# Performance work log

Measured on AMD Instinct MI355X. Metric: run time of the kernel, lower is better.

## Reference

```python
import jax, jax.numpy as jnp
import numpy as np
import math

C_S, C_Z = 384, 128
N_HEAD, C = 12, 16
N_QP, N_PV = 4, 8
B, N_RES = 1, 384


def quat_to_rot(q):
    # q: (..., 4) unnormalized quaternion -> (..., 3, 3) rotation matrix
    q = q / jnp.linalg.norm(q, axis=-1, keepdims=True)
    w, x, y, z = q[..., 0], q[..., 1], q[..., 2], q[..., 3]
    R = jnp.stack([
        1 - 2 * (y * y + z * z), 2 * (x * y - w * z), 2 * (x * z + w * y),
        2 * (x * y + w * z), 1 - 2 * (x * x + z * z), 2 * (y * z - w * x),
        2 * (x * z - w * y), 2 * (y * z + w * x), 1 - 2 * (x * x + y * y),
    ], axis=-1)
    return R.reshape(q.shape[:-1] + (3, 3))


def warp_3d_point(T, p):
    # T: (..., 1, 1, N, 4, 4) rigid transforms; p: (..., H, P, N, 3)
    R = T[..., :3, :3]
    t = T[..., :3, 3]
    return jnp.squeeze(R @ p[..., None], -1) + t


def warp_3d_point_inv(T, p):
    # Inverse rigid transform: R^T (p - t)
    R = T[..., :3, :3]
    t = T[..., :3, 3]
    return jnp.squeeze(jnp.swapaxes(R, -1, -2) @ (p - t)[..., None], -1)


def setup_inputs() -> dict:
    key = jax.random.key(0)
    ks = jax.random.split(key, 24)
    s = jax.random.normal(ks[0], (B, N_RES, C_S), dtype=jnp.float32)
    z = jax.random.normal(ks[1], (B, N_RES, N_RES, C_Z), dtype=jnp.float32)
    # Build rigid backbone transforms T (rotation from random quaternion + translation)
    quat = jax.random.normal(ks[2], (B, N_RES, 4), dtype=jnp.float32)
    trans = jax.random.normal(ks[3], (B, N_RES, 3), dtype=jnp.float32) * 10.0
    R = quat_to_rot(quat)
    T = jnp.zeros((B, N_RES, 4, 4), dtype=jnp.float32)
    T = T.at[..., :3, :3].set(R)
    T = T.at[..., :3, 3].set(trans)
    T = T.at[..., 3, 3].set(1.0)

    def lin(k, din, dout):
        kw, kb = jax.random.split(k)
        W = jax.random.normal(kw, (din, dout), dtype=jnp.float32) * 0.02
        b = jax.random.normal(kb, (dout,), dtype=jnp.float32) * 0.01
        return W, b

    Wq, bq = lin(ks[4], C_S, N_HEAD * C)
    Wk, bk = lin(ks[5], C_S, N_HEAD * C)
    Wv, bv = lin(ks[6], C_S, N_HEAD * C)
    Wqp, bqp = lin(ks[7], C_S, 3 * N_QP * N_HEAD)
    Wkp, bkp = lin(ks[8], C_S, 3 * N_QP * N_HEAD)
    Wvp, bvp = lin(ks[9], C_S, 3 * N_PV * N_HEAD)
    Wb, bb = lin(ks[10], C_Z, N_HEAD)
    d_out_in = N_HEAD * C_Z + N_HEAD * C + N_HEAD * 4 * N_PV
    Wo, bo = lin(ks[11], d_out_in, C_S)
    head_weights = jax.random.normal(ks[12], (N_HEAD,), dtype=jnp.float32) * 0.1
    return dict(s=s, z=z, T=T, Wq=Wq, bq=bq, Wk=Wk, bk=bk, Wv=Wv, bv=bv,
                Wqp=Wqp, bqp=bqp, Wkp=Wkp, bkp=bkp, Wvp=Wvp, bvp=bvp,
                Wb=Wb, bb=bb, Wo=Wo, bo=bo, head_weights=head_weights)


def ipa_forward(s, z, T, Wq, bq, Wk, bk, Wv, bv, Wqp, bqp, Wkp, bkp,
                Wvp, bvp, Wb, bb, Wo, bo, head_weights):
    batch = s.shape[:-2]
    n = s.shape[-2]
    # --- prepare qkv ---
    def heads(x):  # (..., N, H*C) -> (..., H, N, C)
        return jnp.moveaxis(x.reshape(batch + (n, N_HEAD, C)), -3, -2)
    q = heads(s @ Wq + bq)
    k = heads(s @ Wk + bk)
    v = heads(s @ Wv + bv)

    def pts(x, P):  # (..., N, 3*H*P) -> (..., H, P, N, 3)
        x = x.reshape(batch + (n, 3, N_HEAD, P))
        return jnp.moveaxis(x, (-4, -3), (-2, -1))
    qp = pts(s @ Wqp + bqp, N_QP)
    kp = pts(s @ Wkp + bkp, N_QP)
    vp = pts(s @ Wvp + bvp, N_PV)

    # --- attention scores (Alg 22 line 7) ---
    wc = math.sqrt(2.0 / (9.0 * N_QP))
    wl = math.sqrt(1.0 / 3.0)
    gamma = jax.nn.softplus(head_weights).reshape(-1, 1, 1)  # (H,1,1)
    q = q * (1.0 / math.sqrt(C))
    bias = jnp.moveaxis(z @ Wb + bb, -1, -3)  # (..., H, N, N)
    qk = jnp.einsum('...hic,...hjc->...hij', q, k)
    T_bc = T.reshape(batch + (1, 1, n, 4, 4))
    tqp = warp_3d_point(T_bc, qp)[..., :, None, :]   # (..., H, QP, N, 1, 3)
    tkp = warp_3d_point(T_bc, kp)[..., None, :, :]   # (..., H, QP, 1, N, 3)
    sq_dist = jnp.sum((tqp - tkp) ** 2, axis=-1)      # (..., H, QP, N, N)
    qpkp_term = gamma * (wc / 2.0) * jnp.sum(sq_dist, axis=-3)  # (..., H, N, N)
    att = jax.nn.softmax(wl * (qk + bias - qpkp_term), axis=-1)

    # --- outputs ---
    pairwise = jnp.einsum('...ijc,...hij->...hic', z, att)
    pairwise = jnp.moveaxis(pairwise, -3, -2).reshape(batch + (n, N_HEAD * C_Z))
    v_out = jnp.einsum('...hij,...hjc->...hic', att, v)
    v_out = jnp.moveaxis(v_out, -3, -2).reshape(batch + (n, N_HEAD * C))
    vt = warp_3d_point(T_bc, vp)                                # (..., H, PV, N, 3)
    v_att = jnp.einsum('...hij,...hkjp->...hkip', att, vt)     # (..., H, PV, N, 3)
    v_tr = warp_3d_point_inv(T_bc, v_att)                       # (..., H, PV, N, 3)
    v_tr = jnp.einsum('...hpic->...ichp', v_tr)                 # (..., N, 3, H, PV)
    norm = jnp.linalg.norm(v_tr, axis=-3, keepdims=True)        # (..., N, 1, H, PV)
    vp_norm = norm.reshape(batch + (n, N_HEAD * N_PV))
    vp_out = v_tr.reshape(batch + (n, 3 * N_HEAD * N_PV))

    out = jnp.concatenate([v_out, vp_out, vp_norm, pairwise], axis=-1)
    return out @ Wo + bo


def reference(s, z, T, Wq, bq, Wk, bk, Wv, bv, Wqp, bqp, Wkp, bkp,
              Wvp, bvp, Wb, bb, Wo, bo, head_weights):
    return ipa_forward(s, z, T, Wq, bq, Wk, bk, Wv, bv, Wqp, bqp, Wkp, bkp,
                       Wvp, bvp, Wb, bb, Wo, bo, head_weights)
```

## Files before the change

### kernel.cpp

```cpp
#include <hip/hip_runtime.h>
#include <math.h>

#define NRES 384
#define NH   12
#define WLc 0.5773502691896258f
#define WCc 0.23570226039551587f

typedef __attribute__((ext_vector_type(8))) _Float16 half8;
typedef __attribute__((ext_vector_type(2))) _Float16 half2v;
typedef __attribute__((ext_vector_type(4))) float f32x4;

#define OFF_P    0
#define OFF_SH   442368
#define OFF_WCT  516096
#define OFF_BCT  737280
#define OFF_QE   738432
#define OFF_KE   885888
#define OFF_VET  1033344
#define OFF_WOT  1143936
#define OFF_CAT  1549440
#define OFF_ATT  1954944
#define OFF_BIAS 2839680

__global__ __launch_bounds__(256) void pack_bias(
    const float* __restrict__ s,  const float* __restrict__ z,
    const float* __restrict__ Wq,  const float* __restrict__ bq,
    const float* __restrict__ Wk,  const float* __restrict__ bk,
    const float* __restrict__ Wv,  const float* __restrict__ bv,
    const float* __restrict__ Wqp, const float* __restrict__ bqp,
    const float* __restrict__ Wkp, const float* __restrict__ bkp,
    const float* __restrict__ Wvp, const float* __restrict__ bvp,
    const float* __restrict__ Wb,  const float* __restrict__ bb,
    const float* __restrict__ Wo,
    float* __restrict__ ws)
{
    int b = blockIdx.x, t = threadIdx.x;
    __shared__ float tile[64 * 65];
    __shared__ _Float16 wbT[16 * 136];
    __shared__ float sbb[16];

    if (b >= 451) {
        _Float16* biasb = (_Float16*)(ws + OFF_BIAS);
        int bi = b - 451;
        size_t m0 = (size_t)bi * 64;
        if (t < 128) {
            #pragma unroll
            for (int h = 0; h < 12; h++) wbT[h * 136 + t] = (_Float16)(WLc * Wb[t * 12 + h]);
            #pragma unroll
            for (int h = 12; h < 16; h++) wbT[h * 136 + t] = (_Float16)0.f;
        }
        if (t < 16) sbb[t] = (t < 12) ? WLc * bb[t] : 0.f;
        __syncthreads();
        int w = t >> 6, lane = t & 63;
        int m = lane & 15, q = lane >> 4;
        size_t ri = m0 + w * 16 + m;
        const float* zr = z + ri * 128 + q * 8;
        f32x4 acc = {0};
        #pragma unroll
        for (int sI = 0; sI < 4; sI++) {
            float4 v0 = *(const float4*)(zr + sI * 32);
            float4 v1 = *(const float4*)(zr + sI * 32 + 4);
            half8 a;
            a[0]=(_Float16)v0.x; a[1]=(_Float16)v0.y; a[2]=(_Float16)v0.z; a[3]=(_Float16)v0.w;
            a[4]=(_Float16)v1.x; a[5]=(_Float16)v1.y; a[6]=(_Float16)v1.z; a[7]=(_Float16)v1.w;
            half8 bf = *(const half8*)(wbT + m * 136 + sI * 32 + q * 8);
            acc = __builtin_amdgcn_mfma_f32_16x16x32_f16(a, bf, acc, 0, 0, 0);
        }
        if (m < 12) {
            #pragma unroll
            for (int r = 0; r < 4; r++)
                biasb[(size_t)m * 147456 + m0 + w * 16 + q * 4 + r] = (_Float16)(acc[r] + sbb[m]);
        }
        return;
    }

    _Float16* sh  = (_Float16*)(ws + OFF_SH);
    _Float16* wct = (_Float16*)(ws + OFF_WCT);
    _Float16* wot = (_Float16*)(ws + OFF_WOT);
    float* bct = ws + OFF_BCT;

    if (b < 144) {
        int id = b * 256 + t;
        float4 v = ((const float4*)s)[id];
        _Float16 r[4] = { (_Float16)v.x, (_Float16)v.y, (_Float16)v.z, (_Float16)v.w };
        *(uint2*)(sh + id * 4) = *(uint2*)r;
        return;
    }
    if (b < 252) {
        int ti = b - 144;
        int k0 = (ti % 6) * 64, n0 = (ti / 6) * 64;
        int cl = t & 63, rg = t >> 6;
        int ncat = n0 + cl;
        const float* W; int dout, col;
        if      (ncat < 192) { W = Wq;  dout = 192; col = ncat; }
        else if (ncat < 384) { W = Wk;  dout = 192; col = ncat - 192; }
        else if (ncat < 576) { W = Wv;  dout = 192; col = ncat - 384; }
        else if (ncat < 720) { W = Wqp; dout = 144; col = ncat - 576; }
        else if (ncat < 864) { W = Wkp; dout = 144; col = ncat - 720; }
        else                 { W = Wvp; dout = 288; col = ncat - 864; }
        #pragma unroll
        for (int u = 0; u < 16; u++) {
            int r = rg * 16 + u;
            tile[r * 65 + cl] = W[(size_t)(k0 + r) * dout + col];
        }
        __syncthreads();
        #pragma unroll
        for (int u2 = 0; u2 < 2; u2++) {
            int item = t + 256 * u2;
            int nl = item >> 3, kg = item & 7;
            half8 rr;
            #pragma unroll
            for (int jj = 0; jj < 8; jj++) rr[jj] = (_Float16)tile[(kg * 8 + jj) * 65 + nl];
            *(half8*)(wct + (size_t)(n0 + nl) * 384 + k0 + kg * 8) = rr;
        }
        return;
    }
    if (b < 450) {
        int ti = b - 252;
        int k0 = (ti % 33) * 64, n0 = (ti / 33) * 64;
        int cl = t & 63, rg = t >> 6;
        #pragma unroll
        for (int u = 0; u < 16; u++) {
            int r = rg * 16 + u;
            tile[r * 65 + cl] = Wo[(size_t)(k0 + r) * 384 + n0 + cl];
        }
        __syncthreads();
        #pragma unroll
        for (int u2 = 0; u2 < 2; u2++) {
            int item = t + 256 * u2;
            int nl = item >> 3, kg = item & 7;
            half8 rr;
            #pragma unroll
            for (int jj = 0; jj < 8; jj++) rr[jj] = (_Float16)tile[(kg * 8 + jj) * 65 + nl];
            *(half8*)(wot + (size_t)(n0 + nl) * 2112 + k0 + kg * 8) = rr;
        }
        return;
    }
    for (int e = t; e < 1152; e += 256) {
        float bv_;
        if      (e < 192) bv_ = bq[e];
        else if (e < 384) bv_ = bk[e - 192];
        else if (e < 576) bv_ = bv[e - 384];
        else if (e < 720) bv_ = bqp[e - 576];
        else if (e < 864) bv_ = bkp[e - 720];
        else              bv_ = bvp[e - 864];
        bct[e] = bv_;
    }
}

__global__ __launch_bounds__(256) void proj_mfma(float* __restrict__ ws)
{
    const _Float16* sh  = (const _Float16*)(ws + OFF_SH);
    const _Float16* wct = (const _Float16*)(ws + OFF_WCT);
    const float* bct = ws + OFF_BCT;
    float* P = ws + OFF_P;

    __shared__ float sAcc[2][16][65];

    int t = threadIdx.x, w = t >> 6, lane = t & 63;
    int m = lane & 15, q = lane >> 4;
    int mh = w & 1, kh = w >> 1;
    int n0 = blockIdx.x * 64, m0 = blockIdx.y * 32 + mh * 16;

    f32x4 acc[4] = {0};
    const _Float16* arow = sh + (size_t)(m0 + m) * 384 + kh * 192;
    #pragma unroll 3
    for (int s = 0; s < 6; s++) {
        int k = s * 32 + q * 8;
        half8 a = *(const half8*)(arow + k);
        #pragma unroll
        for (int nt = 0; nt < 4; nt++) {
            half8 b = *(const half8*)(wct + (size_t)(n0 + nt * 16 + m) * 384 + kh * 192 + k);
            acc[nt] = __builtin_amdgcn_mfma_f32_16x16x32_f16(a, b, acc[nt], 0, 0, 0);
        }
    }
    if (kh == 0) {
        #pragma unroll
        for (int nt = 0; nt < 4; nt++)
            #pragma unroll
            for (int r = 0; r < 4; r++)
                sAcc[mh][q * 4 + r][nt * 16 + m] = acc[nt][r];
    }
    __syncthreads();
    if (kh == 1) {
        #pragma unroll
        for (int nt = 0; nt < 4; nt++) {
            int col = n0 + nt * 16 + m;
            float bias = bct[col];
            #pragma unroll
            for (int r = 0; r < 4; r++)
                P[(size_t)(m0 + q * 4 + r) * 1152 + col] =
                    acc[nt][r] + sAcc[mh][q * 4 + r][nt * 16 + m] + bias;
        }
    }
}

__global__ __launch_bounds__(192) void prep_kernel(
    const float* __restrict__ T, const float* __restrict__ hw,
    float* __restrict__ ws)
{
    int i = blockIdx.x, t = threadIdx.x;
    const float* pr = ws + OFF_P + (size_t)i * 1152;
    float* Qe = ws + OFF_QE;
    float* Ke = ws + OFF_KE;
    _Float16* vet = (_Float16*)(ws + OFF_VET);

    __shared__ float sT[16], sG[12];
    __shared__ float sTQ[12][4][3], sTK[12][4][3];
    if (t < 16) sT[t] = T[i * 16 + t];
    if (t < 12) { float x = hw[t]; sG[t] = (x > 20.f) ? x : log1pf(__expf(x)); }
    __syncthreads();
    float R00=sT[0],R01=sT[1],R02=sT[2],t0=sT[3];
    float R10=sT[4],R11=sT[5],R12=sT[6],t1=sT[7];
    float R20=sT[8],R21=sT[9],R22=sT[10],t2=sT[11];

    if (t < 48) {
        int h = t >> 2, p = t & 3;
        float a0 = pr[576 + 0*48 + h*4 + p], a1 = pr[576 + 1*48 + h*4 + p], a2 = pr[576 + 2*48 + h*4 + p];
        sTQ[h][p][0] = R00*a0 + R01*a1 + R02*a2 + t0;
        sTQ[h][p][1] = R10*a0 + R11*a1 + R12*a2 + t1;
        sTQ[h][p][2] = R20*a0 + R21*a1 + R22*a2 + t2;
    } else if (t < 96) {
        int tt = t - 48, h = tt >> 2, p = tt & 3;
        float a0 = pr[720 + 0*48 + h*4 + p], a1 = pr[720 + 1*48 + h*4 + p], a2 = pr[720 + 2*48 + h*4 + p];
        sTK[h][p][0] = R00*a0 + R01*a1 + R02*a2 + t0;
        sTK[h][p][1] = R10*a0 + R11*a1 + R12*a2 + t1;
        sTK[h][p][2] = R20*a0 + R21*a1 + R22*a2 + t2;
    } else {
        int tt = t - 96, h = tt >> 3, p = tt & 7;
        float a0 = pr[864 + 0*96 + h*8 + p], a1 = pr[864 + 1*96 + h*8 + p], a2 = pr[864 + 2*96 + h*8 + p];
        vet[(size_t)(h*48 + 16 + p*3 + 0) * 384 + i] = (_Float16)(R00*a0 + R01*a1 + R02*a2 + t0);
        vet[(size_t)(h*48 + 16 + p*3 + 1) * 384 + i] = (_Float16)(R10*a0 + R11*a1 + R12*a2 + t1);
        vet[(size_t)(h*48 + 16 + p*3 + 2) * 384 + i] = (_Float16)(R20*a0 + R21*a1 + R22*a2 + t2);
    }
    {
        int h = t >> 4, c = t & 15;
        vet[(size_t)(h*48 + c) * 384 + i] = (_Float16)pr[384 + h*16 + c];
        if (t < 96) vet[(size_t)((t>>3)*48 + 40 + (t&7)) * 384 + i] = (_Float16)0.f;
        Qe[(size_t)i*384 + h*32 + c] = WLc * 0.25f * pr[h*16 + c];
        Ke[((size_t)h*384 + i)*32 + c] = pr[192 + h*16 + c];
    }
    __syncthreads();
    if (t < 144) {
        int h = t / 12, d = t % 12, p = d / 3, r = d % 3;
        float gw = WLc * sG[h] * WCc;
        Qe[(size_t)i*384 + h*32 + 16 + d] = gw * sTQ[h][p][r];
        Ke[((size_t)h*384 + i)*32 + 16 + d] = sTK[h][p][r];
    }
    if (t < 12) {
        int h = t;
        float sqq = 0.f, sqk = 0.f;
        #pragma unroll
        for (int p = 0; p < 4; p++)
            #pragma unroll
            for (int r = 0; r < 3; r++) { sqq += sTQ[h][p][r]*sTQ[h][p][r]; sqk += sTK[h][p][r]*sTK[h][p][r]; }
        float gw = WLc * sG[h] * WCc;
        Qe[(size_t)i*384 + h*32 + 28] = -0.5f * gw;
        Qe[(size_t)i*384 + h*32 + 29] = -0.5f * gw * sqq;
        Qe[(size_t)i*384 + h*32 + 30] = 0.f;
        Qe[(size_t)i*384 + h*32 + 31] = 0.f;
        Ke[((size_t)h*384 + i)*32 + 28] = sqk;
        Ke[((size_t)h*384 + i)*32 + 29] = 1.f;
        Ke[((size_t)h*384 + i)*32 + 30] = 0.f;
        Ke[((size_t)h*384 + i)*32 + 31] = 0.f;
    }
}

__global__ __launch_bounds__(512) void logits_out40(
    const float* __restrict__ T, float* __restrict__ ws)
{
    __shared__ float sQe[8 * 32];
    __shared__ float sLg[8][384];
    __shared__ float sMS[16];
    __shared__ _Float16 sAttL[8 * 392];
    __shared__ float sO[8 * 49];
    __shared__ float sT8[8 * 16];

    int h = blockIdx.y, i0 = blockIdx.x * 8;
    int t = threadIdx.x;
    const float* Qe = ws + OFF_QE;
    const float* Ke = ws + OFF_KE;
    const _Float16* biasb = (const _Float16*)(ws + OFF_BIAS);
    const _Float16* vet = (const _Float16*)(ws + OFF_VET);
    _Float16* attg = (_Float16*)(ws + OFF_ATT);
    _Float16* catb = (_Float16*)(ws + OFF_CAT);

    if (t < 256)
        sQe[t] = Qe[(size_t)(i0 + (t >> 5)) * 384 + h * 32 + (t & 31)];
    if (t < 128)
        sT8[t] = T[(size_t)(i0 + (t >> 4)) * 16 + (t & 15)];
    __syncthreads();

    float lgv[8];
    if (t < 384) {
        int j = t;
        float ke[32];
        const float4* kr = (const float4*)(Ke + ((size_t)h * 384 + j) * 32);
        #pragma unroll
        for (int u = 0; u < 8; u++) { float4 v = kr[u]; ke[u*4]=v.x; ke[u*4+1]=v.y; ke[u*4+2]=v.z; ke[u*4+3]=v.w; }
        #pragma unroll
        for (int ii = 0; ii < 8; ii++) {
            float acc = (float)biasb[(size_t)h * 147456 + (size_t)(i0 + ii) * 384 + j];
            #pragma unroll
            for (int c = 0; c < 32; c++) acc += sQe[ii * 32 + c] * ke[c];
            lgv[ii] = acc;
            sLg[ii][j] = acc;
        }
    }
    __syncthreads();
    {
        int w = t >> 6, lane = t & 63;
        float vv[6], mx = -1e30f;
        #pragma unroll
        for (int u = 0; u < 6; u++) { vv[u] = sLg[w][lane + 64 * u]; mx = fmaxf(mx, vv[u]); }
        #pragma unroll
        for (int off = 1; off < 64; off <<= 1) mx = fmaxf(mx, __shfl_xor(mx, off));
        float sm = 0.f;
        #pragma unroll
        for (int u = 0; u < 6; u++) sm += __expf(vv[u] - mx);
        #pragma unroll
        for (int off = 1; off < 64; off <<= 1) sm += __shfl_xor(sm, off);
        if (lane == 0) { sMS[w] = mx; sMS[8 + w] = sm; }
    }
    __syncthreads();
    if (t < 384) {
        int j = t;
        #pragma unroll
        for (int ii = 0; ii < 8; ii++) {
            float a = __expf(lgv[ii] - sMS[ii]) * (1.0f / sMS[8 + ii]);
            attg[((size_t)h * 384 + i0 + ii) * 384 + j] = (_Float16)a;
            sAttL[ii * 392 + j] = (_Float16)a;
        }
    }
    __syncthreads();

    int w = t >> 6, lane = t & 63;
    int m16 = lane & 15, q = lane >> 4;
    if (w < 3) {
        int nt = w;
        f32x4 acc = {0};
        #pragma unroll 3
        for (int s = 0; s < 12; s++) {
            int k = s * 32 + q * 8;
            half8 a;
            if (m16 < 8) a = *(const half8*)(sAttL + m16 * 392 + k);
            else         a = (half8){0,0,0,0,0,0,0,0};
            half8 bfr = *(const half8*)(vet + (size_t)(h * 48 + nt * 16 + m16) * 384 + k);
            acc = __builtin_amdgcn_mfma_f32_16x16x32_f16(a, bfr, acc, 0, 0, 0);
        }
        #pragma unroll
        for (int r = 0; r < 4; r++) {
            int row = q * 4 + r;
            if (row < 8) sO[row * 49 + nt * 16 + m16] = acc[r];
        }
    }
    __syncthreads();

    if (t < 128) {
        int il = t >> 4, c = t & 15;
        catb[(size_t)(i0 + il) * 2112 + h * 16 + c] = (_Float16)sO[il * 49 + c];
    }
    if (t < 64) {
        int il = t >> 3, p = t & 7;
        const float* o = sO + il * 49 + 16 + p * 3;
        const float* Ti = sT8 + il * 16;
        float x0 = o[0] - Ti[3], x1 = o[1] - Ti[7], x2 = o[2] - Ti[11];
        float r0 = Ti[0]*x0 + Ti[4]*x1 + Ti[8]*x2;
        float r1 = Ti[1]*x0 + Ti[5]*x1 + Ti[9]*x2;
        float r2 = Ti[2]*x0 + Ti[6]*x1 + Ti[10]*x2;
        _Float16* cr = catb + (size_t)(i0 + il) * 2112;
        cr[192 + 0*96 + h*8 + p] = (_Float16)r0;
        cr[192 + 1*96 + h*8 + p] = (_Float16)r1;
        cr[192 + 2*96 + h*8 + p] = (_Float16)r2;
        cr[480 + h*8 + p] = (_Float16)sqrtf(r0*r0 + r1*r1 + r2*r2);
    }
}

__global__ __launch_bounds__(256) void pairwise_mfma(
    const float* __restrict__ z, float* __restrict__ ws)
{
    __shared__ _Float16 ztT[128 * 136];
    __shared__ __attribute__((aligned(16))) _Float16 sPW[1536];
    int i = blockIdx.x;
    int t = threadIdx.x, w = t >> 6, lane = t & 63;
    int m16 = lane & 15, q = lane >> 4;
    const _Float16* attg = (const _Float16*)(ws + OFF_ATT);
    _Float16* catb = (_Float16*)(ws + OFF_CAT);

    f32x4 acc0 = {0}, acc1 = {0};
    const _Float16* arow = attg + ((size_t)(m16 < 12 ? m16 : 0) * 384 + i) * 384;

    int cq = t & 31, g = t >> 5;
    for (int jc = 0; jc < 3; jc++) {
        if (jc) __syncthreads();
        const float* zb = z + ((size_t)i * 384 + jc * 128) * 128;
        #pragma unroll
        for (int jp = 0; jp < 8; jp++) {
            int j = g * 16 + jp * 2;
            float4 v0 = *(const float4*)(zb + (size_t)j * 128 + cq * 4);
            float4 v1 = *(const float4*)(zb + (size_t)(j + 1) * 128 + cq * 4);
            half2v c0 = {(_Float16)v0.x, (_Float16)v1.x};
            half2v c1 = {(_Float16)v0.y, (_Float16)v1.y};
            half2v c2 = {(_Float16)v0.z, (_Float16)v1.z};
            half2v c3 = {(_Float16)v0.w, (_Float16)v1.w};
            *(half2v*)(ztT + (cq * 4 + 0) * 136 + j) = c0;
            *(half2v*)(ztT + (cq * 4 + 1) * 136 + j) = c1;
            *(half2v*)(ztT + (cq * 4 + 2) * 136 + j) = c2;
            *(half2v*)(ztT + (cq * 4 + 3) * 136 + j) = c3;
        }
        __syncthreads();
        #pragma unroll
        for (int ks = 0; ks < 4; ks++) {
            int k = ks * 32 + q * 8;
            half8 a;
            if (m16 < 12) a = *(const half8*)(arow + jc * 128 + k);
            else          a = (half8){0,0,0,0,0,0,0,0};
            half8 b0 = *(const half8*)(ztT + (w * 32 + m16) * 136 + k);
            half8 b1 = *(const half8*)(ztT + (w * 32 + 16 + m16) * 136 + k);
            acc0 = __builtin_amdgcn_mfma_f32_16x16x32_f16(a, b0, acc0, 0, 0, 0);
            acc1 = __builtin_amdgcn_mfma_f32_16x16x32_f16(a, b1, acc1, 0, 0, 0);
        }
    }
    if (q < 3) {
        #pragma unroll
        for (int r = 0; r < 4; r++) {
            int h = q * 4 + r;
            sPW[h * 128 + w * 32 + m16]      = (_Float16)acc0[r];
            sPW[h * 128 + w * 32 + 16 + m16] = (_Float16)acc1[r];
        }
    }
    __syncthreads();
    if (t < 192)
        *(half8*)(catb + (size_t)i * 2112 + 576 + t * 8) = *(const half8*)(sPW + t * 8);
}

__global__ __launch_bounds__(256) void outgemm_mfma(
    float* __restrict__ ws, const float* __restrict__ bo, float* __restrict__ out)
{
    const _Float16* catb = (const _Float16*)(ws + OFF_CAT);
    const _Float16* wot = (const _Float16*)(ws + OFF_WOT);

    __shared__ float sAcc[2][16][65];

    int t = threadIdx.x, w = t >> 6, lane = t & 63;
    int m = lane & 15, q = lane >> 4;
    int mh = w & 1, kh = w >> 1;
    int n0 = blockIdx.x * 64;
    int m0 = blockIdx.y * 32 + mh * 16;

    f32x4 acc[4] = {0};
    int row = m0 + m;
    const _Float16* ar = catb + (size_t)row * 2112 + kh * 1056;
    #pragma unroll 3
    for (int s = 0; s < 33; s++) {
        int k = s * 32 + q * 8;
        half8 a = *(const half8*)(ar + k);
        #pragma unroll
        for (int nt = 0; nt < 4; nt++) {
            half8 b = *(const half8*)(wot + (size_t)(n0 + nt * 16 + m) * 2112 + kh * 1056 + k);
            acc[nt] = __builtin_amdgcn_mfma_f32_16x16x32_f16(a, b, acc[nt], 0, 0, 0);
        }
    }
    if (kh == 0) {
        #pragma unroll
        for (int nt = 0; nt < 4; nt++)
            #pragma unroll
            for (int r = 0; r < 4; r++)
                sAcc[mh][q * 4 + r][nt * 16 + m] = acc[nt][r];
    }
    __syncthreads();
    if (kh == 1) {
        #pragma unroll
        for (int nt = 0; nt < 4; nt++) {
            int col = n0 + nt * 16 + m;
            float bv = bo[col];
            #pragma unroll
            for (int r = 0; r < 4; r++)
                out[(size_t)(m0 + q * 4 + r) * 384 + col] =
                    acc[nt][r] + sAcc[mh][q * 4 + r][nt * 16 + m] + bv;
        }
    }
}

extern "C" void kernel_launch(void* const* d_in, const int* in_sizes, int n_in,
                              void* d_out, int out_size, void* d_ws, size_t ws_size,
                              hipStream_t stream)
{
    const float* s   = (const float*)d_in[0];
    const float* z   = (const float*)d_in[1];
    const float* T   = (const float*)d_in[2];
    const float* Wq  = (const float*)d_in[3];
    const float* bq  = (const float*)d_in[4];
    const float* Wk  = (const float*)d_in[5];
    const float* bk  = (const float*)d_in[6];
    const float* Wv  = (const float*)d_in[7];
    const float* bv  = (const float*)d_in[8];
    const float* Wqp = (const float*)d_in[9];
    const float* bqp = (const float*)d_in[10];
    const float* Wkp = (const float*)d_in[11];
    const float* bkp = (const float*)d_in[12];
    const float* Wvp = (const float*)d_in[13];
    const float* bvp = (const float*)d_in[14];
    const float* Wb  = (const float*)d_in[15];
    const float* bb  = (const float*)d_in[16];
    const float* Wo  = (const float*)d_in[17];
    const float* bo  = (const float*)d_in[18];
    const float* hw  = (const float*)d_in[19];
    float* ws  = (float*)d_ws;
    float* out = (float*)d_out;

    pack_bias<<<2755, 256, 0, stream>>>(s, z, Wq, bq, Wk, bk, Wv, bv,
                                        Wqp, bqp, Wkp, bkp, Wvp, bvp, Wb, bb, Wo, ws);
    proj_mfma<<<dim3(18, 12), 256, 0, stream>>>(ws);
    prep_kernel<<<384, 192, 0, stream>>>(T, hw, ws);
    logits_out40<<<dim3(48, 12), 512, 0, stream>>>(T, ws);
    pairwise_mfma<<<384, 256, 0, stream>>>(z, ws);
    outgemm_mfma<<<dim3(6, 12), 256, 0, stream>>>(ws, bo, out);
}
```

Measured before the change: 215.0 us.

## Fuse bias, logits, softmax, value and pairwise stages into one per-row kernel

```diff
diff --git a/kernel.cpp b/kernel.cpp
--- a/kernel.cpp
+++ b/kernel.cpp
@@ -19,60 +19,20 @@
 #define OFF_VET  1033344
 #define OFF_WOT  1143936
 #define OFF_CAT  1549440
-#define OFF_ATT  1954944
-#define OFF_BIAS 2839680
-
-__global__ __launch_bounds__(256) void pack_bias(
-    const float* __restrict__ s,  const float* __restrict__ z,
+
+__global__ __launch_bounds__(256) void pack_weights(
+    const float* __restrict__ s,
     const float* __restrict__ Wq,  const float* __restrict__ bq,
     const float* __restrict__ Wk,  const float* __restrict__ bk,
     const float* __restrict__ Wv,  const float* __restrict__ bv,
     const float* __restrict__ Wqp, const float* __restrict__ bqp,
     const float* __restrict__ Wkp, const float* __restrict__ bkp,
     const float* __restrict__ Wvp, const float* __restrict__ bvp,
-    const float* __restrict__ Wb,  const float* __restrict__ bb,
     const float* __restrict__ Wo,
     float* __restrict__ ws)
 {
     int b = blockIdx.x, t = threadIdx.x;
     __shared__ float tile[64 * 65];
-    __shared__ _Float16 wbT[16 * 136];
-    __shared__ float sbb[16];
-
-    if (b >= 451) {
-        _Float16* biasb = (_Float16*)(ws + OFF_BIAS);
-        int bi = b - 451;
-        size_t m0 = (size_t)bi * 64;
-        if (t < 128) {
-            #pragma unroll
-            for (int h = 0; h < 12; h++) wbT[h * 136 + t] = (_Float16)(WLc * Wb[t * 12 + h]);
-            #pragma unroll
-            for (int h = 12; h < 16; h++) wbT[h * 136 + t] = (_Float16)0.f;
-        }
-        if (t < 16) sbb[t] = (t < 12) ? WLc * bb[t] : 0.f;
-        __syncthreads();
-        int w = t >> 6, lane = t & 63;
-        int m = lane & 15, q = lane >> 4;
-        size_t ri = m0 + w * 16 + m;
-        const float* zr = z + ri * 128 + q * 8;
-        f32x4 acc = {0};
-        #pragma unroll
-        for (int sI = 0; sI < 4; sI++) {
-            float4 v0 = *(const float4*)(zr + sI * 32);
-            float4 v1 = *(const float4*)(zr + sI * 32 + 4);
-            half8 a;
-            a[0]=(_Float16)v0.x; a[1]=(_Float16)v0.y; a[2]=(_Float16)v0.z; a[3]=(_Float16)v0.w;
-            a[4]=(_Float16)v1.x; a[5]=(_Float16)v1.y; a[6]=(_Float16)v1.z; a[7]=(_Float16)v1.w;
-            half8 bf = *(const half8*)(wbT + m * 136 + sI * 32 + q * 8);
-            acc = __builtin_amdgcn_mfma_f32_16x16x32_f16(a, bf, acc, 0, 0, 0);
-        }
-        if (m < 12) {
-            #pragma unroll
-            for (int r = 0; r < 4; r++)
-                biasb[(size_t)m * 147456 + m0 + w * 16 + q * 4 + r] = (_Float16)(acc[r] + sbb[m]);
-        }
-        return;
-    }
 
     _Float16* sh  = (_Float16*)(ws + OFF_SH);
     _Float16* wct = (_Float16*)(ws + OFF_WCT);
@@ -266,53 +226,102 @@
     }
 }
 
-__global__ __launch_bounds__(512) void logits_out40(
-    const float* __restrict__ T, float* __restrict__ ws)
+__global__ __launch_bounds__(256) void flash_ipa(
+    const float* __restrict__ z, const float* __restrict__ T,
+    const float* __restrict__ Wb, const float* __restrict__ bb,
+    float* __restrict__ ws)
 {
-    __shared__ float sQe[8 * 32];
-    __shared__ float sLg[8][384];
-    __shared__ float sMS[16];
-    __shared__ _Float16 sAttL[8 * 392];
-    __shared__ float sO[8 * 49];
-    __shared__ float sT8[8 * 16];
-
-    int h = blockIdx.y, i0 = blockIdx.x * 8;
-    int t = threadIdx.x;
+    __shared__ __attribute__((aligned(16))) char uB[34816];
+    __shared__ __attribute__((aligned(16))) _Float16 pL[12 * 392];
+    __shared__ _Float16 wbT[16 * 136];
+    __shared__ float sTl[16];
+    __shared__ float sOL[12 * 49];
+    __shared__ __attribute__((aligned(16))) _Float16 sPW[1536];
+
+    float* lgL = (float*)uB;
+    _Float16* ztT = (_Float16*)uB;
+
+    int i = blockIdx.x, t = threadIdx.x;
+    int w = t >> 6, lane = t & 63;
+    int m16 = lane & 15, q = lane >> 4;
+
     const float* Qe = ws + OFF_QE;
     const float* Ke = ws + OFF_KE;
-    const _Float16* biasb = (const _Float16*)(ws + OFF_BIAS);
     const _Float16* vet = (const _Float16*)(ws + OFF_VET);
-    _Float16* attg = (_Float16*)(ws + OFF_ATT);
     _Float16* catb = (_Float16*)(ws + OFF_CAT);
 
-    if (t < 256)
-        sQe[t] = Qe[(size_t)(i0 + (t >> 5)) * 384 + h * 32 + (t & 31)];
-    if (t < 128)
-        sT8[t] = T[(size_t)(i0 + (t >> 4)) * 16 + (t & 15)];
-    __syncthreads();
-
-    float lgv[8];
-    if (t < 384) {
-        int j = t;
-        float ke[32];
-        const float4* kr = (const float4*)(Ke + ((size_t)h * 384 + j) * 32);
-        #pragma unroll
-        for (int u = 0; u < 8; u++) { float4 v = kr[u]; ke[u*4]=v.x; ke[u*4+1]=v.y; ke[u*4+2]=v.z; ke[u*4+3]=v.w; }
-        #pragma unroll
-        for (int ii = 0; ii < 8; ii++) {
-            float acc = (float)biasb[(size_t)h * 147456 + (size_t)(i0 + ii) * 384 + j];
-            #pragma unroll
-            for (int c = 0; c < 32; c++) acc += sQe[ii * 32 + c] * ke[c];
-            lgv[ii] = acc;
-            sLg[ii][j] = acc;
-        }
-    }
-    __syncthreads();
-    {
-        int w = t >> 6, lane = t & 63;
+    if (t < 16) sTl[t] = T[i * 16 + t];
+    if (t >= 192) {
+        int t2 = t - 192;
+        #pragma unroll
+        for (int cc = 0; cc < 2; cc++) {
+            int col = t2 * 2 + cc;
+            #pragma unroll
+            for (int h = 0; h < 12; h++) wbT[h * 136 + col] = (_Float16)(WLc * Wb[col * 12 + h]);
+            #pragma unroll
+            for (int h = 12; h < 16; h++) wbT[h * 136 + col] = (_Float16)0.f;
+        }
+    }
+
+    if (t < 192) {
+        int j0 = t * 2;
+        float ke0[32], ke1[32];
+        const float4* kr0 = (const float4*)(Ke + ((size_t)0 * 384 + j0) * 32);
+        (void)kr0;
+        const float* qrow = Qe + (size_t)i * 384;
+        #pragma unroll 2
+        for (int h = 0; h < 12; h++) {
+            const float4* k0p = (const float4*)(Ke + ((size_t)h * 384 + j0) * 32);
+            const float4* k1p = (const float4*)(Ke + ((size_t)h * 384 + j0 + 1) * 32);
+            #pragma unroll
+            for (int u = 0; u < 8; u++) {
+                float4 a = k0p[u], b = k1p[u];
+                ke0[u*4]=a.x; ke0[u*4+1]=a.y; ke0[u*4+2]=a.z; ke0[u*4+3]=a.w;
+                ke1[u*4]=b.x; ke1[u*4+1]=b.y; ke1[u*4+2]=b.z; ke1[u*4+3]=b.w;
+            }
+            float bbv = WLc * bb[h];
+            float acc0 = bbv, acc1 = bbv;
+            #pragma unroll
+            for (int c = 0; c < 32; c++) {
+                float qv = qrow[h * 32 + c];
+                acc0 += qv * ke0[c];
+                acc1 += qv * ke1[c];
+            }
+            lgL[h * 392 + j0]     = acc0;
+            lgL[h * 392 + j0 + 1] = acc1;
+        }
+    }
+    __syncthreads();
+
+    #pragma unroll
+    for (int mt = 0; mt < 6; mt++) {
+        int j0 = (w * 6 + mt) * 16;
+        const float* zr = z + ((size_t)i * 384 + j0 + m16) * 128 + q * 8;
+        f32x4 acc = {0};
+        #pragma unroll
+        for (int ks = 0; ks < 4; ks++) {
+            float4 v0 = *(const float4*)(zr + ks * 32);
+            float4 v1 = *(const float4*)(zr + ks * 32 + 4);
+            half8 a;
+            a[0]=(_Float16)v0.x; a[1]=(_Float16)v0.y; a[2]=(_Float16)v0.z; a[3]=(_Float16)v0.w;
+            a[4]=(_Float16)v1.x; a[5]=(_Float16)v1.y; a[6]=(_Float16)v1.z; a[7]=(_Float16)v1.w;
+            half8 bf = *(const half8*)(wbT + m16 * 136 + ks * 32 + q * 8);
+            acc = __builtin_amdgcn_mfma_f32_16x16x32_f16(a, bf, acc, 0, 0, 0);
+        }
+        if (m16 < 12) {
+            float* lp = lgL + m16 * 392 + j0 + q * 4;
+            #pragma unroll
+            for (int r = 0; r < 4; r++) lp[r] += acc[r];
+        }
+    }
+    __syncthreads();
+
+    #pragma unroll
+    for (int rr = 0; rr < 3; rr++) {
+        int row = w * 3 + rr;
         float vv[6], mx = -1e30f;
         #pragma unroll
-        for (int u = 0; u < 6; u++) { vv[u] = sLg[w][lane + 64 * u]; mx = fmaxf(mx, vv[u]); }
+        for (int u = 0; u < 6; u++) { vv[u] = lgL[row * 392 + lane + 64 * u]; mx = fmaxf(mx, vv[u]); }
         #pragma unroll
         for (int off = 1; off < 64; off <<= 1) mx = fmaxf(mx, __shfl_xor(mx, off));
         float sm = 0.f;
@@ -320,79 +329,48 @@
         for (int u = 0; u < 6; u++) sm += __expf(vv[u] - mx);
         #pragma unroll
         for (int off = 1; off < 64; off <<= 1) sm += __shfl_xor(sm, off);
-        if (lane == 0) { sMS[w] = mx; sMS[8 + w] = sm; }
-    }
-    __syncthreads();
-    if (t < 384) {
-        int j = t;
-        #pragma unroll
-        for (int ii = 0; ii < 8; ii++) {
-            float a = __expf(lgv[ii] - sMS[ii]) * (1.0f / sMS[8 + ii]);
-            attg[((size_t)h * 384 + i0 + ii) * 384 + j] = (_Float16)a;
-            sAttL[ii * 392 + j] = (_Float16)a;
-        }
-    }
-    __syncthreads();
-
-    int w = t >> 6, lane = t & 63;
-    int m16 = lane & 15, q = lane >> 4;
-    if (w < 3) {
-        int nt = w;
-        f32x4 acc = {0};
-        #pragma unroll 3
-        for (int s = 0; s < 12; s++) {
-            int k = s * 32 + q * 8;
-            half8 a;
-            if (m16 < 8) a = *(const half8*)(sAttL + m16 * 392 + k);
-            else         a = (half8){0,0,0,0,0,0,0,0};
-            half8 bfr = *(const half8*)(vet + (size_t)(h * 48 + nt * 16 + m16) * 384 + k);
-            acc = __builtin_amdgcn_mfma_f32_16x16x32_f16(a, bfr, acc, 0, 0, 0);
-        }
-        #pragma unroll
-        for (int r = 0; r < 4; r++) {
-            int row = q * 4 + r;
-            if (row < 8) sO[row * 49 + nt * 16 + m16] = acc[r];
-        }
-    }
-    __syncthreads();
-
-    if (t < 128) {
-        int il = t >> 4, c = t & 15;
-        catb[(size_t)(i0 + il) * 2112 + h * 16 + c] = (_Float16)sO[il * 49 + c];
-    }
-    if (t < 64) {
-        int il = t >> 3, p = t & 7;
-        const float* o = sO + il * 49 + 16 + p * 3;
-        const float* Ti = sT8 + il * 16;
-        float x0 = o[0] - Ti[3], x1 = o[1] - Ti[7], x2 = o[2] - Ti[11];
-        float r0 = Ti[0]*x0 + Ti[4]*x1 + Ti[8]*x2;
-        float r1 = Ti[1]*x0 + Ti[5]*x1 + Ti[9]*x2;
-        float r2 = Ti[2]*x0 + Ti[6]*x1 + Ti[10]*x2;
-        _Float16* cr = catb + (size_t)(i0 + il) * 2112;
-        cr[192 + 0*96 + h*8 + p] = (_Float16)r0;
-        cr[192 + 1*96 + h*8 + p] = (_Float16)r1;
-        cr[192 + 2*96 + h*8 + p] = (_Float16)r2;
-        cr[480 + h*8 + p] = (_Float16)sqrtf(r0*r0 + r1*r1 + r2*r2);
-    }
-}
-
-__global__ __launch_bounds__(256) void pairwise_mfma(
-    const float* __restrict__ z, float* __restrict__ ws)
-{
-    __shared__ _Float16 ztT[128 * 136];
-    __shared__ __attribute__((aligned(16))) _Float16 sPW[1536];
-    int i = blockIdx.x;
-    int t = threadIdx.x, w = t >> 6, lane = t & 63;
-    int m16 = lane & 15, q = lane >> 4;
-    const _Float16* attg = (const _Float16*)(ws + OFF_ATT);
-    _Float16* catb = (_Float16*)(ws + OFF_CAT);
+        float inv = 1.0f / sm;
+        #pragma unroll
+        for (int u = 0; u < 6; u++)
+            pL[row * 392 + lane + 64 * u] = (_Float16)(__expf(vv[u] - mx) * inv);
+    }
+    __syncthreads();
+
+    {
+        f32x4 oa[3][3] = {};
+        #pragma unroll
+        for (int kk = 0; kk < 12; kk++) {
+            int k = kk * 32 + q * 8;
+            half8 bfr;
+            if (m16 < 12) bfr = *(const half8*)(pL + m16 * 392 + k);
+            else          bfr = (half8){0,0,0,0,0,0,0,0};
+            #pragma unroll
+            for (int hh = 0; hh < 3; hh++) {
+                int h = w * 3 + hh;
+                #pragma unroll
+                for (int mt = 0; mt < 3; mt++) {
+                    half8 a = *(const half8*)(vet + (size_t)(h * 48 + mt * 16 + m16) * 384 + k);
+                    oa[hh][mt] = __builtin_amdgcn_mfma_f32_16x16x32_f16(a, bfr, oa[hh][mt], 0, 0, 0);
+                }
+            }
+        }
+        #pragma unroll
+        for (int hh = 0; hh < 3; hh++) {
+            int h = w * 3 + hh;
+            if (m16 == h) {
+                #pragma unroll
+                for (int mt = 0; mt < 3; mt++)
+                    #pragma unroll
+                    for (int r = 0; r < 4; r++)
+                        sOL[h * 49 + mt * 16 + q * 4 + r] = oa[hh][mt][r];
+            }
+        }
+    }
 
     f32x4 acc0 = {0}, acc1 = {0};
-    const _Float16* arow = attg + ((size_t)(m16 < 12 ? m16 : 0) * 384 + i) * 384;
-
     int cq = t & 31, g = t >> 5;
     for (int jc = 0; jc < 3; jc++) {
-        if (jc) __syncthreads();
+        __syncthreads();
         const float* zb = z + ((size_t)i * 384 + jc * 128) * 128;
         #pragma unroll
         for (int jp = 0; jp < 8; jp++) {
@@ -413,7 +391,7 @@
         for (int ks = 0; ks < 4; ks++) {
             int k = ks * 32 + q * 8;
             half8 a;
-            if (m16 < 12) a = *(const half8*)(arow + jc * 128 + k);
+            if (m16 < 12) a = *(const half8*)(pL + m16 * 392 + jc * 128 + k);
             else          a = (half8){0,0,0,0,0,0,0,0};
             half8 b0 = *(const half8*)(ztT + (w * 32 + m16) * 136 + k);
             half8 b1 = *(const half8*)(ztT + (w * 32 + 16 + m16) * 136 + k);
@@ -430,8 +408,25 @@
         }
     }
     __syncthreads();
-    if (t < 192)
-        *(half8*)(catb + (size_t)i * 2112 + 576 + t * 8) = *(const half8*)(sPW + t * 8);
+
+    _Float16* cr = catb + (size_t)i * 2112;
+    if (t < 192) {
+        *(half8*)(cr + 576 + t * 8) = *(const half8*)(sPW + t * 8);
+        int h = t >> 4, c = t & 15;
+        cr[h * 16 + c] = (_Float16)sOL[h * 49 + c];
+    }
+    if (t < 96) {
+        int h = t >> 3, p = t & 7;
+        const float* o = sOL + h * 49 + 16 + p * 3;
+        float x0 = o[0] - sTl[3], x1 = o[1] - sTl[7], x2 = o[2] - sTl[11];
+        float r0 = sTl[0]*x0 + sTl[4]*x1 + sTl[8]*x2;
+        float r1 = sTl[1]*x0 + sTl[5]*x1 + sTl[9]*x2;
+        float r2 = sTl[2]*x0 + sTl[6]*x1 + sTl[10]*x2;
+        cr[192 + 0*96 + h*8 + p] = (_Float16)r0;
+        cr[192 + 1*96 + h*8 + p] = (_Float16)r1;
+        cr[192 + 2*96 + h*8 + p] = (_Float16)r2;
+        cr[480 + h*8 + p] = (_Float16)sqrtf(r0*r0 + r1*r1 + r2*r2);
+    }
 }
 
 __global__ __launch_bounds__(256) void outgemm_mfma(
@@ -509,11 +504,10 @@
     float* ws  = (float*)d_ws;
     float* out = (float*)d_out;
 
-    pack_bias<<<2755, 256, 0, stream>>>(s, z, Wq, bq, Wk, bk, Wv, bv,
-                                        Wqp, bqp, Wkp, bkp, Wvp, bvp, Wb, bb, Wo, ws);
+    pack_weights<<<451, 256, 0, stream>>>(s, Wq, bq, Wk, bk, Wv, bv,
+                                          Wqp, bqp, Wkp, bkp, Wvp, bvp, Wo, ws);
     proj_mfma<<<dim3(18, 12), 256, 0, stream>>>(ws);
     prep_kernel<<<384, 192, 0, stream>>>(T, hw, ws);
-    logits_out40<<<dim3(48, 12), 512, 0, stream>>>(T, ws);
-    pairwise_mfma<<<384, 256, 0, stream>>>(z, ws);
+    flash_ipa<<<384, 256, 0, stream>>>(z, T, Wb, bb, ws);
     outgemm_mfma<<<dim3(6, 12), 256, 0, stream>>>(ws, bo, out);
 }
```

Result: slower. 255.0 us (+18.6%).

## Emit transposed fp16 z in bias kernel and reuse it in pairwise GEMM

Applied to the files above, without the earlier changes.

```diff
diff --git a/kernel.cpp b/kernel.cpp
--- a/kernel.cpp
+++ b/kernel.cpp
@@ -7,7 +7,6 @@
 #define WCc 0.23570226039551587f
 
 typedef __attribute__((ext_vector_type(8))) _Float16 half8;
-typedef __attribute__((ext_vector_type(2))) _Float16 half2v;
 typedef __attribute__((ext_vector_type(4))) float f32x4;
 
 #define OFF_P    0
@@ -21,6 +20,7 @@
 #define OFF_CAT  1549440
 #define OFF_ATT  1954944
 #define OFF_BIAS 2839680
+#define OFF_Z16  3724416
 
 __global__ __launch_bounds__(256) void pack_bias(
     const float* __restrict__ s,  const float* __restrict__ z,
@@ -38,11 +38,14 @@
     __shared__ float tile[64 * 65];
     __shared__ _Float16 wbT[16 * 136];
     __shared__ float sbb[16];
+    __shared__ _Float16 zL[64 * 136];
 
     if (b >= 451) {
         _Float16* biasb = (_Float16*)(ws + OFF_BIAS);
+        _Float16* z16t  = (_Float16*)(ws + OFF_Z16);
         int bi = b - 451;
         size_t m0 = (size_t)bi * 64;
+        int ib = bi / 6, j0 = (bi % 6) * 64;
         if (t < 128) {
             #pragma unroll
             for (int h = 0; h < 12; h++) wbT[h * 136 + t] = (_Float16)(WLc * Wb[t * 12 + h]);
@@ -63,8 +66,24 @@
             half8 a;
             a[0]=(_Float16)v0.x; a[1]=(_Float16)v0.y; a[2]=(_Float16)v0.z; a[3]=(_Float16)v0.w;
             a[4]=(_Float16)v1.x; a[5]=(_Float16)v1.y; a[6]=(_Float16)v1.z; a[7]=(_Float16)v1.w;
+            *(half8*)(zL + (w * 16 + m) * 136 + sI * 32 + q * 8) = a;
             half8 bf = *(const half8*)(wbT + m * 136 + sI * 32 + q * 8);
             acc = __builtin_amdgcn_mfma_f32_16x16x32_f16(a, bf, acc, 0, 0, 0);
+        }
+        __syncthreads();
+        {
+            int c = t & 127, jh = t >> 7;
+            _Float16 vals[32];
+            #pragma unroll
+            for (int u = 0; u < 32; u++) vals[u] = zL[(jh * 32 + u) * 136 + c];
+            _Float16* dst = z16t + ((size_t)ib * 128 + c) * 384 + j0 + jh * 32;
+            #pragma unroll
+            for (int g = 0; g < 4; g++) {
+                half8 r;
+                #pragma unroll
+                for (int u = 0; u < 8; u++) r[u] = vals[g * 8 + u];
+                *(half8*)(dst + g * 8) = r;
+            }
         }
         if (m < 12) {
             #pragma unroll
@@ -376,50 +395,30 @@
     }
 }
 
-__global__ __launch_bounds__(256) void pairwise_mfma(
-    const float* __restrict__ z, float* __restrict__ ws)
-{
-    __shared__ _Float16 ztT[128 * 136];
+__global__ __launch_bounds__(256) void pairwise_mfma(float* __restrict__ ws)
+{
     __shared__ __attribute__((aligned(16))) _Float16 sPW[1536];
     int i = blockIdx.x;
     int t = threadIdx.x, w = t >> 6, lane = t & 63;
     int m16 = lane & 15, q = lane >> 4;
     const _Float16* attg = (const _Float16*)(ws + OFF_ATT);
+    const _Float16* z16t = (const _Float16*)(ws + OFF_Z16);
     _Float16* catb = (_Float16*)(ws + OFF_CAT);
 
     f32x4 acc0 = {0}, acc1 = {0};
-    const _Float16* arow = attg + ((size_t)(m16 < 12 ? m16 : 0) * 384 + i) * 384;
-
-    int cq = t & 31, g = t >> 5;
-    for (int jc = 0; jc < 3; jc++) {
-        if (jc) __syncthreads();
-        const float* zb = z + ((size_t)i * 384 + jc * 128) * 128;
-        #pragma unroll
-        for (int jp = 0; jp < 8; jp++) {
-            int j = g * 16 + jp * 2;
-            float4 v0 = *(const float4*)(zb + (size_t)j * 128 + cq * 4);
-            float4 v1 = *(const float4*)(zb + (size_t)(j + 1) * 128 + cq * 4);
-            half2v c0 = {(_Float16)v0.x, (_Float16)v1.x};
-            half2v c1 = {(_Float16)v0.y, (_Float16)v1.y};
-            half2v c2 = {(_Float16)v0.z, (_Float16)v1.z};
-            half2v c3 = {(_Float16)v0.w, (_Float16)v1.w};
-            *(half2v*)(ztT + (cq * 4 + 0) * 136 + j) = c0;
-            *(half2v*)(ztT + (cq * 4 + 1) * 136 + j) = c1;
-            *(half2v*)(ztT + (cq * 4 + 2) * 136 + j) = c2;
-            *(half2v*)(ztT + (cq * 4 + 3) * 136 + j) = c3;
-        }
-        __syncthreads();
-        #pragma unroll
-        for (int ks = 0; ks < 4; ks++) {
-            int k = ks * 32 + q * 8;
-            half8 a;
-            if (m16 < 12) a = *(const half8*)(arow + jc * 128 + k);
-            else          a = (half8){0,0,0,0,0,0,0,0};
-            half8 b0 = *(const half8*)(ztT + (w * 32 + m16) * 136 + k);
-            half8 b1 = *(const half8*)(ztT + (w * 32 + 16 + m16) * 136 + k);
-            acc0 = __builtin_amdgcn_mfma_f32_16x16x32_f16(a, b0, acc0, 0, 0, 0);
-            acc1 = __builtin_amdgcn_mfma_f32_16x16x32_f16(a, b1, acc1, 0, 0, 0);
-        }
+    const _Float16* arow  = attg + ((size_t)(m16 < 12 ? m16 : 0) * 384 + i) * 384;
+    const _Float16* zrow0 = z16t + ((size_t)i * 128 + w * 32 + m16) * 384;
+    const _Float16* zrow1 = zrow0 + 16 * 384;
+    #pragma unroll 4
+    for (int ks = 0; ks < 12; ks++) {
+        int k = ks * 32 + q * 8;
+        half8 a;
+        if (m16 < 12) a = *(const half8*)(arow + k);
+        else          a = (half8){0,0,0,0,0,0,0,0};
+        half8 b0 = *(const half8*)(zrow0 + k);
+        half8 b1 = *(const half8*)(zrow1 + k);
+        acc0 = __builtin_amdgcn_mfma_f32_16x16x32_f16(a, b0, acc0, 0, 0, 0);
+        acc1 = __builtin_amdgcn_mfma_f32_16x16x32_f16(a, b1, acc1, 0, 0, 0);
     }
     if (q < 3) {
         #pragma unroll
@@ -514,6 +513,6 @@
     proj_mfma<<<dim3(18, 12), 256, 0, stream>>>(ws);
     prep_kernel<<<384, 192, 0, stream>>>(T, hw, ws);
     logits_out40<<<dim3(48, 12), 512, 0, stream>>>(T, ws);
-    pairwise_mfma<<<384, 256, 0, stream>>>(z, ws);
+    pairwise_mfma<<<384, 256, 0, stream>>>(ws);
     outgemm_mfma<<<dim3(6, 12), 256, 0, stream>>>(ws, bo, out);
 }
```

Result: slower. 223.7 us (+4.1%).
